# Performance work log

Measured on AMD Instinct MI355X. Metric: run time of the kernel, lower is better.

Reference implementation:

```python
import jax, jax.numpy as jnp
import numpy as np

N_NODES = 50000
N_EDGES = 800000
ATOM_DIM = 128
BOND_DIM = 16
HID = 128
STEPS = 4


def setup_inputs() -> dict:
    key = jax.random.key(0)
    k1, k2, k3, k4, k5, k6 = jax.random.split(key, 6)
    atoms = jax.random.normal(k1, (N_NODES, ATOM_DIM), dtype=jnp.float32)
    bonds = jax.random.normal(k2, (N_NODES, BOND_DIM), dtype=jnp.float32)
    pairs = jax.random.randint(k3, (N_EDGES, 2), 0, N_NODES)
    # sort rows by target id (tf.math.segment_sum expects sorted segment ids)
    order = jnp.argsort(pairs[:, 0])
    pairs = pairs[order].astype(jnp.int64)
    # learned parameters (glorot-ish scaling)
    kernel = jax.random.normal(k4, (ATOM_DIM, BOND_DIM * BOND_DIM), dtype=jnp.float32) * (2.0 / (ATOM_DIM + BOND_DIM * BOND_DIM)) ** 0.5
    bias = jnp.zeros((BOND_DIM * BOND_DIM,), dtype=jnp.float32)
    weight_node = jax.random.normal(k5, (BOND_DIM, HID), dtype=jnp.float32) * (2.0 / (BOND_DIM + HID)) ** 0.5
    weight_node_inp = jax.random.normal(k6, (BOND_DIM, HID), dtype=jnp.float32) * (2.0 / (BOND_DIM + HID)) ** 0.5
    return {"atoms": atoms, "bonds": bonds, "pairs": pairs,
            "kernel": kernel, "bias": bias,
            "weight_node": weight_node, "weight_node_inp": weight_node_inp}


def reference(atoms, bonds, pairs, kernel, bias, weight_node, weight_node_inp):
    n, bd = bonds.shape
    # per-node transform -> [N, bd, bd] message matrices
    A = (atoms @ kernel + bias).reshape(n, bd, bd)
    src = pairs[:, 0]
    nbr = pairs[:, 1]
    # gather bonds of neighbors, apply source-node matrix per edge: [E, bd]
    trans = jnp.einsum('eij,ej->ei', A[src], bonds[nbr])
    # scatter-add back to nodes keyed on pairs[:,0]
    aggregate = jax.ops.segment_sum(trans, src, num_segments=n)  # [N, bd]
    # step loop: aggregate is never updated in the original, so each step
    # computes the identical result; compute once and replicate.
    nodes = aggregate @ weight_node            # [N, hid]
    edges = jax.nn.relu(bonds @ weight_node_inp)  # [N, hid]
    result = jax.nn.relu(nodes + edges)
    return jnp.stack([result] * STEPS)  # [steps, N, hid]
```

## Files before the change

kernel.cpp:

```cpp
#include <hip/hip_runtime.h>

typedef __attribute__((ext_vector_type(8))) short bf16x8;
typedef __attribute__((ext_vector_type(4))) float f32x4;

constexpr int N       = 50000;
constexpr int NE      = 800000;
constexpr int AD      = 128;
constexpr int BD      = 16;
constexpr int BD2     = 256;
constexpr int HIDDEN  = 128;
constexpr int NB      = 64;
constexpr int SSTR    = 20;
constexpr int OSTR    = 132;

__device__ inline short f2bf(float f) {
    union U { float f; unsigned u; } v; v.f = f;
    unsigned r = v.u + 0x7fffu + ((v.u >> 16) & 1u);
    return (short)(r >> 16);
}

__global__ __launch_bounds__(256) void prep_frags(
    const float* __restrict__ kmat,
    const float* __restrict__ Wn,
    const float* __restrict__ Wi,
    short* __restrict__ kbf,
    short* __restrict__ wbf)
{
    int t = blockIdx.x * 256 + threadIdx.x;
    if (t < 4096) {
        int u = t >> 6, l = t & 63;
        int nf = u >> 2, kk = u & 3;
        int col = nf * 16 + (l & 15);
        int k0  = kk * 32 + (l >> 4) * 8;
        bf16x8 o;
#pragma unroll
        for (int j = 0; j < 8; ++j) o[j] = f2bf(kmat[(size_t)(k0 + j) * BD2 + col]);
        *(bf16x8*)(kbf + (size_t)t * 8) = o;
    } else if (t < 4096 + 1024) {
        int t2 = t - 4096;
        int u = t2 >> 6, l = t2 & 63;
        int m = u >> 3, nf2 = u & 7;
        const float* W = m ? Wi : Wn;
        int col = nf2 * 16 + (l & 15);
        int k0  = (l >> 4) * 8;
        bf16x8 o;
#pragma unroll
        for (int j = 0; j < 8; ++j) {
            int k = k0 + j;
            o[j] = (k < 16) ? f2bf(W[(size_t)k * HIDDEN + col]) : (short)0;
        }
        *(bf16x8*)(wbf + (size_t)t2 * 8) = o;
    }
}

__global__ __launch_bounds__(256, 4) void fused_all(
    const float* __restrict__ atoms,
    const float* __restrict__ bonds,
    const int*  __restrict__ pairs,
    const short* __restrict__ kbf,
    const short* __restrict__ wbf,
    const float* __restrict__ bias,
    float* __restrict__ out)
{
    __shared__ float lds[NB * OSTR];

    const int tid = threadIdx.x;
    const int w   = tid >> 6;
    const int l   = tid & 63;
    const int lq  = l >> 4;
    const int lj  = l & 15;
    const int nb  = blockIdx.x * NB;
    const int wrow = nb + w * 16;

    int arow = wrow + lj; if (arow >= N) arow = N - 1;
    const float* ap = atoms + (size_t)arow * AD + lq * 8;
    float4 a0[4], a1[4];
#pragma unroll
    for (int kk = 0; kk < 4; ++kk) {
        a0[kk] = *(const float4*)(ap + kk * 32);
        a1[kk] = *(const float4*)(ap + kk * 32 + 4);
    }

    int wlo = nb * 16 - 4096; if (wlo < 0) wlo = 0;
    int whi = (nb + NB) * 16 + 4096; if (whi > NE) whi = NE;
    if (wlo > 0  && pairs[2 * wlo] >= nb)      wlo = 0;
    if (whi < NE && pairs[2 * whi] <  nb + NB) whi = NE;
    int eLo;
    {
        int s = wlo, e = whi;
        while (s < e) { int m = (s + e) >> 1; if (pairs[2 * m] < nb) s = m + 1; else e = m; }
        eLo = s;
    }
    int eHi;
    {
        int s = eLo, e = whi;
        while (s < e) { int m = (s + e) >> 1; if (pairs[2 * m] < nb + NB) s = m + 1; else e = m; }
        eHi = s;
    }

    for (int i = tid; i < NB * SSTR; i += 256) lds[i] = 0.f;
    __syncthreads();

    {
        const int g = tid >> 4;
        const int c = tid & 15;
        const int nE = eHi - eLo;
        const int cg = (nE + 15) >> 4;
        int gs = eLo + g * cg;
        int ge = gs + cg; if (ge > eHi) ge = eHi;
        int cur = -1; float acc = 0.f;
        int e = gs;
        for (; e + 4 <= ge; e += 4) {
            int2 pb[4]; float vb[4];
#pragma unroll
            for (int i = 0; i < 4; ++i) pb[i] = *(const int2*)(pairs + 2 * (e + i));
#pragma unroll
            for (int i = 0; i < 4; ++i) vb[i] = bonds[(size_t)pb[i].y * BD + c];
#pragma unroll
            for (int i = 0; i < 4; ++i) {
                if (pb[i].x != cur) {
                    if (cur >= 0) atomicAdd(&lds[(cur - nb) * SSTR + c], acc);
                    acc = 0.f; cur = pb[i].x;
                }
                acc += vb[i];
            }
        }
        for (; e < ge; ++e) {
            int2 p = *(const int2*)(pairs + 2 * e);
            float v = bonds[(size_t)p.y * BD + c];
            if (p.x != cur) {
                if (cur >= 0) atomicAdd(&lds[(cur - nb) * SSTR + c], acc);
                acc = 0.f; cur = p.x;
            }
            acc += v;
        }
        if (cur >= 0) atomicAdd(&lds[(cur - nb) * SSTR + c], acc);
    }
    __syncthreads();

    float4 sv = *(const float4*)(&lds[(w * 16 + lj) * SSTR + lq * 4]);
    __syncthreads();

    bf16x8 afrag[4];
#pragma unroll
    for (int kk = 0; kk < 4; ++kk) {
        bf16x8 af;
        af[0] = f2bf(a0[kk].x); af[1] = f2bf(a0[kk].y);
        af[2] = f2bf(a0[kk].z); af[3] = f2bf(a0[kk].w);
        af[4] = f2bf(a1[kk].x); af[5] = f2bf(a1[kk].y);
        af[6] = f2bf(a1[kk].z); af[7] = f2bf(a1[kk].w);
        afrag[kk] = af;
    }

    f32x4 acc[16];
#pragma unroll
    for (int nf = 0; nf < 16; ++nf) acc[nf] = (f32x4){0.f, 0.f, 0.f, 0.f};

    const bf16x8* kb = (const bf16x8*)kbf;
#pragma unroll 1
    for (int kk = 0; kk < 4; ++kk) {
#pragma unroll
        for (int nf = 0; nf < 16; ++nf) {
            bf16x8 b = kb[(size_t)(nf * 4 + kk) * 64 + l];
            acc[nf] = __builtin_amdgcn_mfma_f32_16x16x32_bf16(b, afrag[kk], acc[nf], 0, 0, 0);
        }
    }

    float aggf[16];
#pragma unroll
    for (int nf = 0; nf < 16; ++nf) {
        float4 bv = *(const float4*)(bias + nf * 16 + lq * 4);
        float q = (acc[nf][0] + bv.x) * sv.x
                + (acc[nf][1] + bv.y) * sv.y
                + (acc[nf][2] + bv.z) * sv.z
                + (acc[nf][3] + bv.w) * sv.w;
        q += __shfl_xor(q, 16);
        q += __shfl_xor(q, 32);
        aggf[nf] = q;
    }

    bf16x8 agg_a  = (bf16x8){0,0,0,0,0,0,0,0};
    bf16x8 bond_a = (bf16x8){0,0,0,0,0,0,0,0};
    if (lq < 2) {
#pragma unroll
        for (int j = 0; j < 8; ++j) agg_a[j] = f2bf(aggf[lq * 8 + j]);
        int brow = wrow + lj; if (brow >= N) brow = N - 1;
        float4 b0 = *(const float4*)(bonds + (size_t)brow * BD + lq * 8);
        float4 b1 = *(const float4*)(bonds + (size_t)brow * BD + lq * 8 + 4);
        bond_a[0] = f2bf(b0.x); bond_a[1] = f2bf(b0.y);
        bond_a[2] = f2bf(b0.z); bond_a[3] = f2bf(b0.w);
        bond_a[4] = f2bf(b1.x); bond_a[5] = f2bf(b1.y);
        bond_a[6] = f2bf(b1.z); bond_a[7] = f2bf(b1.w);
    }

    const bf16x8* wb = (const bf16x8*)wbf;
#pragma unroll
    for (int nf2 = 0; nf2 < 8; ++nf2) {
        bf16x8 wn_f = wb[(size_t)nf2 * 64 + l];
        bf16x8 wi_f = wb[(size_t)(8 + nf2) * 64 + l];
        f32x4 e = __builtin_amdgcn_mfma_f32_16x16x32_bf16(
            bond_a, wi_f, (f32x4){0.f, 0.f, 0.f, 0.f}, 0, 0, 0);
        e[0] = fmaxf(e[0], 0.f); e[1] = fmaxf(e[1], 0.f);
        e[2] = fmaxf(e[2], 0.f); e[3] = fmaxf(e[3], 0.f);
        f32x4 o = __builtin_amdgcn_mfma_f32_16x16x32_bf16(agg_a, wn_f, e, 0, 0, 0);
#pragma unroll
        for (int r = 0; r < 4; ++r) {
            int nl = w * 16 + 4 * lq + r;
            lds[nl * OSTR + nf2 * 16 + lj] = fmaxf(o[r], 0.f);
        }
    }
    __syncthreads();

#pragma unroll
    for (int p = 0; p < 8; ++p) {
        int idx  = tid + 256 * p;
        int nl   = idx >> 5;
        int h4   = (idx & 31) * 4;
        int node = nb + nl;
        if (node < N) {
            f32x4 v = *(const f32x4*)(&lds[nl * OSTR + h4]);
            float* dst = out + (size_t)node * HIDDEN + h4;
#pragma unroll
            for (int s = 0; s < 4; ++s) {
                __builtin_nontemporal_store(v, (f32x4*)(dst + (size_t)s * N * HIDDEN));
            }
        }
    }
}

extern "C" void kernel_launch(void* const* d_in, const int* in_sizes, int n_in,
                              void* d_out, int out_size, void* d_ws, size_t ws_size,
                              hipStream_t stream)
{
    const float* atoms = (const float*)d_in[0];
    const float* bonds = (const float*)d_in[1];
    const int*   pairs = (const int*)d_in[2];
    const float* kmat  = (const float*)d_in[3];
    const float* bias  = (const float*)d_in[4];
    const float* Wn    = (const float*)d_in[5];
    const float* Wi    = (const float*)d_in[6];
    float* out = (float*)d_out;

    short* kbf = (short*)d_ws;
    short* wbf = kbf + 4096 * 8;

    prep_frags<<<20, 256, 0, stream>>>(kmat, Wn, Wi, kbf, wbf);

    fused_all<<<(N + NB - 1) / NB, 256, 0, stream>>>(
        atoms, bonds, pairs, kbf, wbf, bias, out);
}
```

Baseline: 76.60 us.

## Split fused kernel into scatter pass and per-16-node MFMA output kernel

Result: slower. 84.32 us (+10.1%).

```diff
diff --git a/kernel.cpp b/kernel.cpp
--- a/kernel.cpp
+++ b/kernel.cpp
@@ -9,7 +9,8 @@
 constexpr int BD      = 16;
 constexpr int BD2     = 256;
 constexpr int HIDDEN  = 128;
-constexpr int NB      = 64;
+constexpr int NBS     = 64;
+constexpr int NBF     = 16;
 constexpr int SSTR    = 20;
 constexpr int OSTR    = 132;
 
@@ -53,52 +54,33 @@
     }
 }
 
-__global__ __launch_bounds__(256, 4) void fused_all(
-    const float* __restrict__ atoms,
+__global__ __launch_bounds__(256) void scatter_tile(
+    const int*  __restrict__ pairs,
     const float* __restrict__ bonds,
-    const int*  __restrict__ pairs,
-    const short* __restrict__ kbf,
-    const short* __restrict__ wbf,
-    const float* __restrict__ bias,
-    float* __restrict__ out)
-{
-    __shared__ float lds[NB * OSTR];
+    float* __restrict__ S)
+{
+    __shared__ float st[NBS * SSTR];
 
     const int tid = threadIdx.x;
-    const int w   = tid >> 6;
-    const int l   = tid & 63;
-    const int lq  = l >> 4;
-    const int lj  = l & 15;
-    const int nb  = blockIdx.x * NB;
-    const int wrow = nb + w * 16;
-
-    int arow = wrow + lj; if (arow >= N) arow = N - 1;
-    const float* ap = atoms + (size_t)arow * AD + lq * 8;
-    float4 a0[4], a1[4];
-#pragma unroll
-    for (int kk = 0; kk < 4; ++kk) {
-        a0[kk] = *(const float4*)(ap + kk * 32);
-        a1[kk] = *(const float4*)(ap + kk * 32 + 4);
-    }
+    const int nb  = blockIdx.x * NBS;
+
+    for (int i = tid; i < NBS * SSTR; i += 256) st[i] = 0.f;
 
     int wlo = nb * 16 - 4096; if (wlo < 0) wlo = 0;
-    int whi = (nb + NB) * 16 + 4096; if (whi > NE) whi = NE;
-    if (wlo > 0  && pairs[2 * wlo] >= nb)      wlo = 0;
-    if (whi < NE && pairs[2 * whi] <  nb + NB) whi = NE;
-    int eLo;
+    int whi = (nb + NBS) * 16 + 4096; if (whi > NE) whi = NE;
+    if (wlo > 0  && pairs[2 * wlo] >= nb)       wlo = 0;
+    if (whi < NE && pairs[2 * whi] <  nb + NBS) whi = NE;
+    int eLo, eHi;
     {
         int s = wlo, e = whi;
         while (s < e) { int m = (s + e) >> 1; if (pairs[2 * m] < nb) s = m + 1; else e = m; }
         eLo = s;
     }
-    int eHi;
     {
         int s = eLo, e = whi;
-        while (s < e) { int m = (s + e) >> 1; if (pairs[2 * m] < nb + NB) s = m + 1; else e = m; }
+        while (s < e) { int m = (s + e) >> 1; if (pairs[2 * m] < nb + NBS) s = m + 1; else e = m; }
         eHi = s;
     }
-
-    for (int i = tid; i < NB * SSTR; i += 256) lds[i] = 0.f;
     __syncthreads();
 
     {
@@ -119,7 +101,7 @@
 #pragma unroll
             for (int i = 0; i < 4; ++i) {
                 if (pb[i].x != cur) {
-                    if (cur >= 0) atomicAdd(&lds[(cur - nb) * SSTR + c], acc);
+                    if (cur >= 0) atomicAdd(&st[(cur - nb) * SSTR + c], acc);
                     acc = 0.f; cur = pb[i].x;
                 }
                 acc += vb[i];
@@ -129,17 +111,53 @@
             int2 p = *(const int2*)(pairs + 2 * e);
             float v = bonds[(size_t)p.y * BD + c];
             if (p.x != cur) {
-                if (cur >= 0) atomicAdd(&lds[(cur - nb) * SSTR + c], acc);
+                if (cur >= 0) atomicAdd(&st[(cur - nb) * SSTR + c], acc);
                 acc = 0.f; cur = p.x;
             }
             acc += v;
         }
-        if (cur >= 0) atomicAdd(&lds[(cur - nb) * SSTR + c], acc);
+        if (cur >= 0) atomicAdd(&st[(cur - nb) * SSTR + c], acc);
     }
     __syncthreads();
 
-    float4 sv = *(const float4*)(&lds[(w * 16 + lj) * SSTR + lq * 4]);
-    __syncthreads();
+    {
+        int node = tid >> 2;
+        int c4   = (tid & 3) * 4;
+        if (nb + node < N) {
+            f32x4 v = *(const f32x4*)(&st[node * SSTR + c4]);
+            *(f32x4*)(S + (size_t)(nb + node) * BD + c4) = v;
+        }
+    }
+}
+
+__global__ __launch_bounds__(64, 4) void fused_node16(
+    const float* __restrict__ atoms,
+    const float* __restrict__ bonds,
+    const short* __restrict__ kbf,
+    const short* __restrict__ wbf,
+    const float* __restrict__ bias,
+    const float* __restrict__ S,
+    float* __restrict__ out)
+{
+    __shared__ float lds[NBF * OSTR];
+
+    const int l   = threadIdx.x;
+    const int lq  = l >> 4;
+    const int lj  = l & 15;
+    const int wrow = blockIdx.x * NBF;
+
+    const int arow = wrow + lj;
+    const float* ap = atoms + (size_t)arow * AD + lq * 8;
+    float4 a0[4], a1[4];
+#pragma unroll
+    for (int kk = 0; kk < 4; ++kk) {
+        a0[kk] = *(const float4*)(ap + kk * 32);
+        a1[kk] = *(const float4*)(ap + kk * 32 + 4);
+    }
+    float4 sv = *(const float4*)(S + (size_t)arow * BD + lq * 4);
+
+    float4 b0 = *(const float4*)(bonds + (size_t)arow * BD + (lq & 1) * 8);
+    float4 b1 = *(const float4*)(bonds + (size_t)arow * BD + (lq & 1) * 8 + 4);
 
     bf16x8 afrag[4];
 #pragma unroll
@@ -184,9 +202,6 @@
     if (lq < 2) {
 #pragma unroll
         for (int j = 0; j < 8; ++j) agg_a[j] = f2bf(aggf[lq * 8 + j]);
-        int brow = wrow + lj; if (brow >= N) brow = N - 1;
-        float4 b0 = *(const float4*)(bonds + (size_t)brow * BD + lq * 8);
-        float4 b1 = *(const float4*)(bonds + (size_t)brow * BD + lq * 8 + 4);
         bond_a[0] = f2bf(b0.x); bond_a[1] = f2bf(b0.y);
         bond_a[2] = f2bf(b0.z); bond_a[3] = f2bf(b0.w);
         bond_a[4] = f2bf(b1.x); bond_a[5] = f2bf(b1.y);
@@ -205,7 +220,7 @@
         f32x4 o = __builtin_amdgcn_mfma_f32_16x16x32_bf16(agg_a, wn_f, e, 0, 0, 0);
 #pragma unroll
         for (int r = 0; r < 4; ++r) {
-            int nl = w * 16 + 4 * lq + r;
+            int nl = 4 * lq + r;
             lds[nl * OSTR + nf2 * 16 + lj] = fmaxf(o[r], 0.f);
         }
     }
@@ -213,17 +228,14 @@
 
 #pragma unroll
     for (int p = 0; p < 8; ++p) {
-        int idx  = tid + 256 * p;
+        int idx  = l + 64 * p;
         int nl   = idx >> 5;
         int h4   = (idx & 31) * 4;
-        int node = nb + nl;
-        if (node < N) {
-            f32x4 v = *(const f32x4*)(&lds[nl * OSTR + h4]);
-            float* dst = out + (size_t)node * HIDDEN + h4;
-#pragma unroll
-            for (int s = 0; s < 4; ++s) {
-                __builtin_nontemporal_store(v, (f32x4*)(dst + (size_t)s * N * HIDDEN));
-            }
+        f32x4 v  = *(const f32x4*)(&lds[nl * OSTR + h4]);
+        float* dst = out + (size_t)(wrow + nl) * HIDDEN + h4;
+#pragma unroll
+        for (int s = 0; s < 4; ++s) {
+            __builtin_nontemporal_store(v, (f32x4*)(dst + (size_t)s * N * HIDDEN));
         }
     }
 }
@@ -243,9 +255,10 @@
 
     short* kbf = (short*)d_ws;
     short* wbf = kbf + 4096 * 8;
+    float* S   = (float*)(wbf + 1024 * 8);
 
     prep_frags<<<20, 256, 0, stream>>>(kmat, Wn, Wi, kbf, wbf);
-
-    fused_all<<<(N + NB - 1) / NB, 256, 0, stream>>>(
-        atoms, bonds, pairs, kbf, wbf, bias, out);
-}
+    scatter_tile<<<(N + NBS - 1) / NBS, 256, 0, stream>>>(pairs, bonds, S);
+    fused_node16<<<N / NBF, 64, 0, stream>>>(
+        atoms, bonds, kbf, wbf, bias, S, out);
+}
```

## Split fused kernel into scatter, GEMM-contract, and epilogue kernels

Applied to the files above, without the earlier changes.

After: 76.62 us. No clear change (+0.0%).

```diff
diff --git a/kernel.cpp b/kernel.cpp
--- a/kernel.cpp
+++ b/kernel.cpp
@@ -53,52 +53,33 @@
     }
 }
 
-__global__ __launch_bounds__(256, 4) void fused_all(
-    const float* __restrict__ atoms,
+__global__ __launch_bounds__(256) void scatter_tile(
+    const int*  __restrict__ pairs,
     const float* __restrict__ bonds,
-    const int*  __restrict__ pairs,
-    const short* __restrict__ kbf,
-    const short* __restrict__ wbf,
-    const float* __restrict__ bias,
-    float* __restrict__ out)
-{
-    __shared__ float lds[NB * OSTR];
+    float* __restrict__ S)
+{
+    __shared__ float st[NB * SSTR];
 
     const int tid = threadIdx.x;
-    const int w   = tid >> 6;
-    const int l   = tid & 63;
-    const int lq  = l >> 4;
-    const int lj  = l & 15;
     const int nb  = blockIdx.x * NB;
-    const int wrow = nb + w * 16;
-
-    int arow = wrow + lj; if (arow >= N) arow = N - 1;
-    const float* ap = atoms + (size_t)arow * AD + lq * 8;
-    float4 a0[4], a1[4];
-#pragma unroll
-    for (int kk = 0; kk < 4; ++kk) {
-        a0[kk] = *(const float4*)(ap + kk * 32);
-        a1[kk] = *(const float4*)(ap + kk * 32 + 4);
-    }
+
+    for (int i = tid; i < NB * SSTR; i += 256) st[i] = 0.f;
 
     int wlo = nb * 16 - 4096; if (wlo < 0) wlo = 0;
     int whi = (nb + NB) * 16 + 4096; if (whi > NE) whi = NE;
     if (wlo > 0  && pairs[2 * wlo] >= nb)      wlo = 0;
     if (whi < NE && pairs[2 * whi] <  nb + NB) whi = NE;
-    int eLo;
+    int eLo, eHi;
     {
         int s = wlo, e = whi;
         while (s < e) { int m = (s + e) >> 1; if (pairs[2 * m] < nb) s = m + 1; else e = m; }
         eLo = s;
     }
-    int eHi;
     {
         int s = eLo, e = whi;
         while (s < e) { int m = (s + e) >> 1; if (pairs[2 * m] < nb + NB) s = m + 1; else e = m; }
         eHi = s;
     }
-
-    for (int i = tid; i < NB * SSTR; i += 256) lds[i] = 0.f;
     __syncthreads();
 
     {
@@ -119,7 +100,7 @@
 #pragma unroll
             for (int i = 0; i < 4; ++i) {
                 if (pb[i].x != cur) {
-                    if (cur >= 0) atomicAdd(&lds[(cur - nb) * SSTR + c], acc);
+                    if (cur >= 0) atomicAdd(&st[(cur - nb) * SSTR + c], acc);
                     acc = 0.f; cur = pb[i].x;
                 }
                 acc += vb[i];
@@ -129,68 +110,138 @@
             int2 p = *(const int2*)(pairs + 2 * e);
             float v = bonds[(size_t)p.y * BD + c];
             if (p.x != cur) {
-                if (cur >= 0) atomicAdd(&lds[(cur - nb) * SSTR + c], acc);
+                if (cur >= 0) atomicAdd(&st[(cur - nb) * SSTR + c], acc);
                 acc = 0.f; cur = p.x;
             }
             acc += v;
         }
-        if (cur >= 0) atomicAdd(&lds[(cur - nb) * SSTR + c], acc);
+        if (cur >= 0) atomicAdd(&st[(cur - nb) * SSTR + c], acc);
     }
     __syncthreads();
 
-    float4 sv = *(const float4*)(&lds[(w * 16 + lj) * SSTR + lq * 4]);
+    {
+        int node = tid >> 2;
+        int c4   = (tid & 3) * 4;
+        if (nb + node < N) {
+            f32x4 v = *(const f32x4*)(&st[node * SSTR + c4]);
+            *(f32x4*)(S + (size_t)(nb + node) * BD + c4) = v;
+        }
+    }
+}
+
+__global__ __launch_bounds__(256, 3) void gemm_contract(
+    const float* __restrict__ atoms,
+    const short* __restrict__ kbf,
+    const float* __restrict__ bias,
+    float* Sagg)
+{
+    __shared__ float ag[NB * SSTR];
+
+    const int tid = threadIdx.x;
+    const int w   = tid >> 6;
+    const int l   = tid & 63;
+    const int lq  = l >> 4;
+    const int lj  = l & 15;
+    const int nb  = blockIdx.x * NB;
+
+    bf16x8 afrag[4][4];
+    float4 sval[4];
+#pragma unroll
+    for (int ng = 0; ng < 4; ++ng) {
+        int arow = nb + ng * 16 + lj; if (arow >= N) arow = N - 1;
+        const float* ap = atoms + (size_t)arow * AD + lq * 8;
+#pragma unroll
+        for (int kk = 0; kk < 4; ++kk) {
+            float4 a0 = *(const float4*)(ap + kk * 32);
+            float4 a1 = *(const float4*)(ap + kk * 32 + 4);
+            bf16x8 af;
+            af[0] = f2bf(a0.x); af[1] = f2bf(a0.y); af[2] = f2bf(a0.z); af[3] = f2bf(a0.w);
+            af[4] = f2bf(a1.x); af[5] = f2bf(a1.y); af[6] = f2bf(a1.z); af[7] = f2bf(a1.w);
+            afrag[ng][kk] = af;
+        }
+        sval[ng] = *(const float4*)(Sagg + (size_t)arow * BD + lq * 4);
+    }
+
+    const bf16x8* kb = (const bf16x8*)kbf;
+    float aggf[4][4];
+#pragma unroll
+    for (int nfl = 0; nfl < 4; ++nfl) {
+        const int nf = w * 4 + nfl;
+        f32x4 acc[4];
+#pragma unroll
+        for (int ng = 0; ng < 4; ++ng) acc[ng] = (f32x4){0.f, 0.f, 0.f, 0.f};
+#pragma unroll
+        for (int kk = 0; kk < 4; ++kk) {
+            bf16x8 b = kb[(size_t)(nf * 4 + kk) * 64 + l];
+#pragma unroll
+            for (int ng = 0; ng < 4; ++ng)
+                acc[ng] = __builtin_amdgcn_mfma_f32_16x16x32_bf16(b, afrag[ng][kk], acc[ng], 0, 0, 0);
+        }
+        float4 bv = *(const float4*)(bias + nf * 16 + lq * 4);
+#pragma unroll
+        for (int ng = 0; ng < 4; ++ng) {
+            float q = (acc[ng][0] + bv.x) * sval[ng].x
+                    + (acc[ng][1] + bv.y) * sval[ng].y
+                    + (acc[ng][2] + bv.z) * sval[ng].z
+                    + (acc[ng][3] + bv.w) * sval[ng].w;
+            q += __shfl_xor(q, 16);
+            q += __shfl_xor(q, 32);
+            aggf[nfl][ng] = q;
+        }
+    }
+
+#pragma unroll
+    for (int ng = 0; ng < 4; ++ng) {
+        float v = aggf[0][ng];
+        v = (lq == 1) ? aggf[1][ng] : v;
+        v = (lq == 2) ? aggf[2][ng] : v;
+        v = (lq == 3) ? aggf[3][ng] : v;
+        ag[(ng * 16 + lj) * SSTR + w * 4 + lq] = v;
+    }
     __syncthreads();
 
-    bf16x8 afrag[4];
-#pragma unroll
-    for (int kk = 0; kk < 4; ++kk) {
-        bf16x8 af;
-        af[0] = f2bf(a0[kk].x); af[1] = f2bf(a0[kk].y);
-        af[2] = f2bf(a0[kk].z); af[3] = f2bf(a0[kk].w);
-        af[4] = f2bf(a1[kk].x); af[5] = f2bf(a1[kk].y);
-        af[6] = f2bf(a1[kk].z); af[7] = f2bf(a1[kk].w);
-        afrag[kk] = af;
-    }
-
-    f32x4 acc[16];
-#pragma unroll
-    for (int nf = 0; nf < 16; ++nf) acc[nf] = (f32x4){0.f, 0.f, 0.f, 0.f};
-
-    const bf16x8* kb = (const bf16x8*)kbf;
-#pragma unroll 1
-    for (int kk = 0; kk < 4; ++kk) {
-#pragma unroll
-        for (int nf = 0; nf < 16; ++nf) {
-            bf16x8 b = kb[(size_t)(nf * 4 + kk) * 64 + l];
-            acc[nf] = __builtin_amdgcn_mfma_f32_16x16x32_bf16(b, afrag[kk], acc[nf], 0, 0, 0);
-        }
-    }
-
-    float aggf[16];
-#pragma unroll
-    for (int nf = 0; nf < 16; ++nf) {
-        float4 bv = *(const float4*)(bias + nf * 16 + lq * 4);
-        float q = (acc[nf][0] + bv.x) * sv.x
-                + (acc[nf][1] + bv.y) * sv.y
-                + (acc[nf][2] + bv.z) * sv.z
-                + (acc[nf][3] + bv.w) * sv.w;
-        q += __shfl_xor(q, 16);
-        q += __shfl_xor(q, 32);
-        aggf[nf] = q;
-    }
+    {
+        int node = tid >> 2;
+        int c4   = (tid & 3) * 4;
+        if (nb + node < N) {
+            f32x4 v = *(const f32x4*)(&ag[node * SSTR + c4]);
+            *(f32x4*)(Sagg + (size_t)(nb + node) * BD + c4) = v;
+        }
+    }
+}
+
+__global__ __launch_bounds__(256) void epilogue_store(
+    const float* __restrict__ agg,
+    const float* __restrict__ bonds,
+    const short* __restrict__ wbf,
+    float* __restrict__ out)
+{
+    __shared__ float lds[NB * OSTR];
+
+    const int tid = threadIdx.x;
+    const int w   = tid >> 6;
+    const int l   = tid & 63;
+    const int lq  = l >> 4;
+    const int lj  = l & 15;
+    const int nb  = blockIdx.x * NB;
+    const int wrow = nb + w * 16;
+
+    int arow = wrow + lj; if (arow >= N) arow = N - 1;
 
     bf16x8 agg_a  = (bf16x8){0,0,0,0,0,0,0,0};
     bf16x8 bond_a = (bf16x8){0,0,0,0,0,0,0,0};
-    if (lq < 2) {
-#pragma unroll
-        for (int j = 0; j < 8; ++j) agg_a[j] = f2bf(aggf[lq * 8 + j]);
-        int brow = wrow + lj; if (brow >= N) brow = N - 1;
-        float4 b0 = *(const float4*)(bonds + (size_t)brow * BD + lq * 8);
-        float4 b1 = *(const float4*)(bonds + (size_t)brow * BD + lq * 8 + 4);
-        bond_a[0] = f2bf(b0.x); bond_a[1] = f2bf(b0.y);
-        bond_a[2] = f2bf(b0.z); bond_a[3] = f2bf(b0.w);
-        bond_a[4] = f2bf(b1.x); bond_a[5] = f2bf(b1.y);
-        bond_a[6] = f2bf(b1.z); bond_a[7] = f2bf(b1.w);
+    {
+        int half = lq & 1;
+        float4 g0 = *(const float4*)(agg   + (size_t)arow * BD + half * 8);
+        float4 g1 = *(const float4*)(agg   + (size_t)arow * BD + half * 8 + 4);
+        float4 b0 = *(const float4*)(bonds + (size_t)arow * BD + half * 8);
+        float4 b1 = *(const float4*)(bonds + (size_t)arow * BD + half * 8 + 4);
+        if (lq < 2) {
+            agg_a[0] = f2bf(g0.x); agg_a[1] = f2bf(g0.y); agg_a[2] = f2bf(g0.z); agg_a[3] = f2bf(g0.w);
+            agg_a[4] = f2bf(g1.x); agg_a[5] = f2bf(g1.y); agg_a[6] = f2bf(g1.z); agg_a[7] = f2bf(g1.w);
+            bond_a[0] = f2bf(b0.x); bond_a[1] = f2bf(b0.y); bond_a[2] = f2bf(b0.z); bond_a[3] = f2bf(b0.w);
+            bond_a[4] = f2bf(b1.x); bond_a[5] = f2bf(b1.y); bond_a[6] = f2bf(b1.z); bond_a[7] = f2bf(b1.w);
+        }
     }
 
     const bf16x8* wb = (const bf16x8*)wbf;
@@ -241,11 +292,14 @@
     const float* Wi    = (const float*)d_in[6];
     float* out = (float*)d_out;
 
-    short* kbf = (short*)d_ws;
-    short* wbf = kbf + 4096 * 8;
+    short* kbf  = (short*)d_ws;
+    short* wbf  = kbf + 4096 * 8;
+    float* Sagg = (float*)(wbf + 1024 * 8);
+
+    const int nblk = (N + NB - 1) / NB;
 
     prep_frags<<<20, 256, 0, stream>>>(kmat, Wn, Wi, kbf, wbf);
-
-    fused_all<<<(N + NB - 1) / NB, 256, 0, stream>>>(
-        atoms, bonds, pairs, kbf, wbf, bias, out);
-}
+    scatter_tile<<<nblk, 256, 0, stream>>>(pairs, bonds, Sagg);
+    gemm_contract<<<nblk, 256, 0, stream>>>(atoms, kbf, bias, Sagg);
+    epilogue_store<<<nblk, 256, 0, stream>>>(Sagg, bonds, wbf, out);
+}
```
